# Kernel tuning notes

Measured on AMD Instinct MI355X. Metric: run time of the kernel, lower is better.

Reference implementation:

```python
import jax, jax.numpy as jnp
import numpy as np

RATE = 5          # negative_sample_rate
A = 1.0           # _a
BP = 1.0          # _b
REP = 1.0         # repulsion_strength
EPS = 1e-4        # clamp in compute_cross_entropy
BATCH = 65536; C = 100; E = 2048; GN = 16; GP = 5; NIDX = 50000


def setup_inputs() -> dict:
    key = jax.random.key(0)
    ks = jax.random.split(key, 12)
    return {
        'edge_to_idx': jax.random.randint(ks[0], (BATCH,), 0, NIDX),
        'edge_from_idx': jax.random.randint(ks[1], (BATCH,), 0, NIDX),
        'embedding_to': jax.random.normal(ks[2], (BATCH, 2), jnp.float32),
        'embedding_from': jax.random.normal(ks[3], (BATCH, 2), jnp.float32),
        'probs': jax.random.uniform(ks[4], (BATCH,), jnp.float32),
        'pred_edge_to': jax.random.normal(ks[5], (BATCH, C), jnp.float32),
        'pred_edge_from': jax.random.normal(ks[6], (BATCH, C), jnp.float32),
        'perm': jax.random.permutation(ks[7], BATCH * RATE),            # torch.randperm
        'error_conf': jnp.sort(jax.random.randint(ks[8], (E,), 0, NIDX)),
        'neg_grid': jax.random.normal(ks[9], (E, GN, 2), jnp.float32),
        'pos_grid': jax.random.normal(ks[10], (E, GP, 2), jnp.float32),
        'distance_list': jax.random.uniform(ks[11], (E,), jnp.float32),
    }


def _q(d):
    # convert_distance_to_probability: 1 / (1 + a * d^(2b))
    return 1.0 / (1.0 + A * d ** (2.0 * BP))


def _ce_attract(p, q):
    return -p * jnp.log(jnp.clip(q, EPS, 1.0))


def _ce_repulse(p, q):
    return -(1.0 - p) * REP * jnp.log(jnp.clip(1.0 - q, EPS, 1.0))


def _match(idx, error_conf):
    # first position in (sorted) error_conf equal to idx, plus hit mask
    pos = jnp.clip(jnp.searchsorted(error_conf, idx), 0, error_conf.shape[0] - 1)
    return pos, (error_conf[pos] == idx)


def reference(edge_to_idx, edge_from_idx, embedding_to, embedding_from, probs,
              pred_edge_to, pred_edge_from, perm, error_conf, neg_grid,
              pos_grid, distance_list):
    f32 = jnp.float32
    # ---- negative sampling (repeat_interleave + randperm) ----
    emb_neg_to = jnp.repeat(embedding_to, RATE, axis=0)         # [B*R,2]
    pred_neg_to = jnp.repeat(pred_edge_to, RATE, axis=0)        # [B*R,C]
    emb_neg_from = jnp.repeat(embedding_from, RATE, axis=0)[perm]
    pred_neg_from = jnp.repeat(pred_edge_from, RATE, axis=0)[perm]
    # filter_neg: keep where NOT (same argmax AND same max-softmax confidence)
    conf_from = jnp.max(jax.nn.softmax(pred_neg_from, axis=1), axis=1)
    conf_to = jnp.max(jax.nn.softmax(pred_neg_to, axis=1), axis=1)
    same = (jnp.argmax(pred_neg_from, axis=1) == jnp.argmax(pred_neg_to, axis=1)) & (conf_from == conf_to)
    m_neg = (~same).astype(f32)                                 # [B*R]
    neg_dist = jnp.linalg.norm(emb_neg_to - emb_neg_from, axis=1)
    neg_cnt = jnp.sum(m_neg)
    neg_mean = jnp.sum(neg_dist * m_neg) / jnp.maximum(neg_cnt, 1.0)
    # ---- positive distances ----
    pos_dist = jnp.linalg.norm(embedding_to - embedding_from, axis=1)  # [B]
    pos_mean = jnp.mean(pos_dist)
    # ---- confidence-grid pairs (vectorized isin/nonzero loops) ----
    g_to, hit_to = _match(edge_to_idx, error_conf)
    g_from, hit_from = _match(edge_from_idx, error_conf)
    m_to = hit_to.astype(f32)
    m_from = hit_from.astype(f32)
    d_cneg_to = jnp.linalg.norm(embedding_to[:, None, :] - neg_grid[g_to], axis=-1)     # [B,GN]
    d_cneg_from = jnp.linalg.norm(embedding_from[:, None, :] - neg_grid[g_from], axis=-1)
    d_cpos_to = jnp.linalg.norm(embedding_from[:, None, :] - pos_grid[g_to], axis=-1)   # [B,GP]
    d_cpos_from = jnp.linalg.norm(embedding_from[:, None, :] - pos_grid[g_from], axis=-1)
    w_pos_to = m_to * (distance_list[g_to] < 0.5).astype(f32)
    w_pos_from = m_from * (distance_list[g_from] < 1.0).astype(f32)
    # ---- UMAP cross entropy over the concatenated (pos, conf_pos, neg, conf_neg) ----
    ce_pos = _ce_attract(probs, _q(pos_dist)) + _ce_repulse(probs, _q(pos_dist))
    sum_ce = jnp.sum(ce_pos)
    sum_ce += jnp.sum(w_pos_to[:, None] * _ce_attract(1.0, _q(d_cpos_to)))
    sum_ce += jnp.sum(w_pos_from[:, None] * _ce_attract(1.0, _q(d_cpos_from)))
    sum_ce += jnp.sum(m_neg * _ce_repulse(0.0, _q(neg_dist)))
    sum_ce += jnp.sum(m_to[:, None] * _ce_repulse(0.0, _q(d_cneg_to)))
    sum_ce += jnp.sum(m_from[:, None] * _ce_repulse(0.0, _q(d_cneg_from)))
    total_cnt = (pos_dist.shape[0] + GP * (jnp.sum(w_pos_to) + jnp.sum(w_pos_from))
                 + neg_cnt + GN * (jnp.sum(m_to) + jnp.sum(m_from)))
    umap_l = sum_ce / jnp.maximum(total_cnt, 1.0)
    umap_l = jnp.where(jnp.isnan(umap_l), 0.0, umap_l)
    # ---- margin loss ----
    is_pred_same = (jnp.argmax(pred_edge_to, axis=1) == jnp.argmax(pred_edge_from, axis=1)).astype(f32)
    batch_margin = pos_mean + (neg_mean - pos_mean) * (1.0 - probs)
    margin = (1.0 - is_pred_same) * batch_margin
    margin_loss = jnp.mean(jax.nn.relu(margin - pos_dist))
    margin_loss = jnp.where(jnp.isnan(margin_loss), 0.0, margin_loss)
    return (umap_l, margin_loss, umap_l + margin_loss)


if __name__ == '__main__':
    out = reference(**setup_inputs())
    print([float(o) for o in out])
```

## Files before the change

### kernel.cpp

```cpp
#include <hip/hip_runtime.h>
#include <math.h>

#define B_SZ   65536
#define RATE   5
#define NNEG   (B_SZ * RATE)
#define NC     100
#define NE     2048
#define GN     16
#define GP     5
#define EPSC   1e-4f

#define NB_NEG 1280
#define NB_POS 256
#define NB_MAR 256


__device__ __forceinline__ double wave_sum(double v) {
    #pragma unroll
    for (int off = 32; off > 0; off >>= 1) v += __shfl_down(v, off, 64);
    return v;
}

__device__ __forceinline__ float clip01(float x) {
    return fminf(fmaxf(x, EPSC), 1.0f);
}

__global__ __launch_bounds__(256, 2) void k_rowstats(
    const float* __restrict__ pred_to, const float* __restrict__ pred_from,
    float* __restrict__ conf_to, float* __restrict__ conf_from,
    unsigned char* __restrict__ am_to, unsigned char* __restrict__ am_from)
{
    int i = blockIdx.x * blockDim.x + threadIdx.x;
    const float* row = (i < B_SZ) ? pred_to + (size_t)i * NC
                                  : pred_from + (size_t)(i - B_SZ) * NC;
    const float4* r4 = (const float4*)row;
    float4 v[25];
    #pragma unroll
    for (int t = 0; t < 25; ++t) v[t] = r4[t];

    float m = -INFINITY;
    #pragma unroll
    for (int t = 0; t < 25; ++t)
        m = fmaxf(m, fmaxf(fmaxf(v[t].x, v[t].y), fmaxf(v[t].z, v[t].w)));

    int bi = NC;
    float s = 0.0f;
    #pragma unroll
    for (int t = 0; t < 25; ++t) {
        float e0 = v[t].x, e1 = v[t].y, e2 = v[t].z, e3 = v[t].w;
        if (e0 == m) bi = min(bi, 4 * t + 0);
        if (e1 == m) bi = min(bi, 4 * t + 1);
        if (e2 == m) bi = min(bi, 4 * t + 2);
        if (e3 == m) bi = min(bi, 4 * t + 3);
        s += expf(e0 - m) + expf(e1 - m) + expf(e2 - m) + expf(e3 - m);
    }
    float conf = 1.0f / s;
    if (i < B_SZ) { conf_to[i] = conf;  am_to[i] = (unsigned char)bi; }
    else { conf_from[i - B_SZ] = conf; am_from[i - B_SZ] = (unsigned char)bi; }
}

__global__ __launch_bounds__(256) void k_negpos(
    const int* __restrict__ perm,
    const float2* __restrict__ emb_to, const float2* __restrict__ emb_from,
    const float* __restrict__ conf_to, const float* __restrict__ conf_from,
    const unsigned char* __restrict__ am_to, const unsigned char* __restrict__ am_from,
    const int* __restrict__ idx_to, const int* __restrict__ idx_from,
    const float* __restrict__ probs,
    const int* __restrict__ error_conf,
    const float2* __restrict__ neg_grid, const float2* __restrict__ pos_grid,
    const float* __restrict__ dist_list,
    double* __restrict__ pneg, double* __restrict__ ppos)
{
    if (blockIdx.x < NB_NEG) {
        int i = blockIdx.x * blockDim.x + threadIdx.x;
        double ce = 0.0, cnt = 0.0, dsum = 0.0;
        {
            int jt = i / RATE;
            int jf = perm[i] / RATE;
            bool same = (am_to[jt] == am_from[jf]) && (conf_to[jt] == conf_from[jf]);
            if (!same) {
                float2 et = emb_to[jt], ef = emb_from[jf];
                float dx = et.x - ef.x, dy = et.y - ef.y;
                float d  = sqrtf(dx * dx + dy * dy);
                float q  = 1.0f / (1.0f + d * d);
                ce   = (double)(-logf(clip01(1.0f - q)));
                cnt  = 1.0;
                dsum = (double)d;
            }
        }
        ce = wave_sum(ce); cnt = wave_sum(cnt); dsum = wave_sum(dsum);
        __shared__ double sr[3][4];
        int w = threadIdx.x >> 6;
        if ((threadIdx.x & 63) == 0) { sr[0][w] = ce; sr[1][w] = cnt; sr[2][w] = dsum; }
        __syncthreads();
        if (threadIdx.x == 0) {
            pneg[blockIdx.x * 3 + 0] = sr[0][0] + sr[0][1] + sr[0][2] + sr[0][3];
            pneg[blockIdx.x * 3 + 1] = sr[1][0] + sr[1][1] + sr[1][2] + sr[1][3];
            pneg[blockIdx.x * 3 + 2] = sr[2][0] + sr[2][1] + sr[2][2] + sr[2][3];
        }
    } else {
        int blk = blockIdx.x - NB_NEG;
        __shared__ int ec[NE];
        for (int t = threadIdx.x; t < NE; t += blockDim.x) ec[t] = error_conf[t];
        __syncthreads();

        int i = blk * blockDim.x + threadIdx.x;
        double v[6] = {0, 0, 0, 0, 0, 0};
        {
            float2 et = emb_to[i], ef = emb_from[i];
            float dx = et.x - ef.x, dy = et.y - ef.y;
            float d  = sqrtf(dx * dx + dy * dy);
            v[1] = (double)d;
            float p = probs[i];
            float q = 1.0f / (1.0f + d * d);
            double ce = (double)(-p * logf(clip01(q)) - (1.0f - p) * logf(clip01(1.0f - q)));

            int vt = idx_to[i];
            int lo = 0, hi = NE;
            while (lo < hi) { int mid = (lo + hi) >> 1; if (ec[mid] < vt) lo = mid + 1; else hi = mid; }
            int gt = (lo < NE) ? lo : NE - 1;
            bool hit_t = (ec[gt] == vt);

            int vf = idx_from[i];
            lo = 0; hi = NE;
            while (lo < hi) { int mid = (lo + hi) >> 1; if (ec[mid] < vf) lo = mid + 1; else hi = mid; }
            int gf = (lo < NE) ? lo : NE - 1;
            bool hit_f = (ec[gf] == vf);

            if (hit_t) {
                v[4] = 1.0;
                double s = 0.0;
                #pragma unroll
                for (int k = 0; k < GN; ++k) {
                    float2 g = neg_grid[gt * GN + k];
                    float ax = et.x - g.x, ay = et.y - g.y;
                    float dd = sqrtf(ax * ax + ay * ay);
                    float qq = 1.0f / (1.0f + dd * dd);
                    s += (double)(-logf(clip01(1.0f - qq)));
                }
                ce += s;
                if (dist_list[gt] < 0.5f) {
                    v[2] = 1.0;
                    double s2 = 0.0;
                    #pragma unroll
                    for (int k = 0; k < GP; ++k) {
                        float2 g = pos_grid[gt * GP + k];
                        float ax = ef.x - g.x, ay = ef.y - g.y;
                        float dd = sqrtf(ax * ax + ay * ay);
                        float qq = 1.0f / (1.0f + dd * dd);
                        s2 += (double)(-logf(clip01(qq)));
                    }
                    ce += s2;
                }
            }
            if (hit_f) {
                v[5] = 1.0;
                double s = 0.0;
                #pragma unroll
                for (int k = 0; k < GN; ++k) {
                    float2 g = neg_grid[gf * GN + k];
                    float ax = ef.x - g.x, ay = ef.y - g.y;
                    float dd = sqrtf(ax * ax + ay * ay);
                    float qq = 1.0f / (1.0f + dd * dd);
                    s += (double)(-logf(clip01(1.0f - qq)));
                }
                ce += s;
                if (dist_list[gf] < 1.0f) {
                    v[3] = 1.0;
                    double s2 = 0.0;
                    #pragma unroll
                    for (int k = 0; k < GP; ++k) {
                        float2 g = pos_grid[gf * GP + k];
                        float ax = ef.x - g.x, ay = ef.y - g.y;
                        float dd = sqrtf(ax * ax + ay * ay);
                        float qq = 1.0f / (1.0f + dd * dd);
                        s2 += (double)(-logf(clip01(qq)));
                    }
                    ce += s2;
                }
            }
            v[0] = ce;
        }
        __shared__ double sr2[6][4];
        int w = threadIdx.x >> 6;
        #pragma unroll
        for (int j = 0; j < 6; ++j) {
            double r = wave_sum(v[j]);
            if ((threadIdx.x & 63) == 0) sr2[j][w] = r;
        }
        __syncthreads();
        if (threadIdx.x < 6) {
            int j = threadIdx.x;
            ppos[blk * 6 + j] = sr2[j][0] + sr2[j][1] + sr2[j][2] + sr2[j][3];
        }
    }
}

__global__ __launch_bounds__(64) void k_reduce1(
    const double* __restrict__ pneg, const double* __restrict__ ppos,
    double* __restrict__ acc)
{
    int lane = threadIdx.x;
    double ce = 0.0, cnt = 0.0, dsum = 0.0;
    for (int b = lane; b < NB_NEG; b += 64) {
        ce   += pneg[b * 3 + 0];
        cnt  += pneg[b * 3 + 1];
        dsum += pneg[b * 3 + 2];
    }
    double pv[6] = {0, 0, 0, 0, 0, 0};
    for (int b = lane; b < NB_POS; b += 64) {
        #pragma unroll
        for (int j = 0; j < 6; ++j) pv[j] += ppos[b * 6 + j];
    }
    ce   = wave_sum(ce);
    cnt  = wave_sum(cnt);
    dsum = wave_sum(dsum);
    #pragma unroll
    for (int j = 0; j < 6; ++j) pv[j] = wave_sum(pv[j]);
    if (lane == 0) {
        acc[0] = ce + pv[0];
        acc[1] = cnt;
        acc[2] = dsum;
        acc[3] = pv[1];
        acc[4] = pv[2];
        acc[5] = pv[3];
        acc[6] = pv[4];
        acc[7] = pv[5];
    }
}

__global__ __launch_bounds__(256) void k_margin(
    const float2* __restrict__ emb_to, const float2* __restrict__ emb_from,
    const float* __restrict__ probs,
    const unsigned char* __restrict__ am_to, const unsigned char* __restrict__ am_from,
    const double* __restrict__ acc,
    double* __restrict__ pmar)
{
    int i = blockIdx.x * blockDim.x + threadIdx.x;
    float pos_mean = (float)(acc[3] / (double)B_SZ);
    float neg_mean = (float)(acc[2] / fmax(acc[1], 1.0));
    double ms;
    {
        float2 et = emb_to[i], ef = emb_from[i];
        float dx = et.x - ef.x, dy = et.y - ef.y;
        float d  = sqrtf(dx * dx + dy * dy);
        float p  = probs[i];
        float bm = pos_mean + (neg_mean - pos_mean) * (1.0f - p);
        float m  = (am_to[i] == am_from[i]) ? 0.0f : bm;
        ms = (double)fmaxf(m - d, 0.0f);
    }
    ms = wave_sum(ms);
    __shared__ double sr[4];
    int w = threadIdx.x >> 6;
    if ((threadIdx.x & 63) == 0) sr[w] = ms;
    __syncthreads();
    if (threadIdx.x == 0) pmar[blockIdx.x] = sr[0] + sr[1] + sr[2] + sr[3];
}

__global__ __launch_bounds__(64) void k_final(
    const double* __restrict__ acc, const double* __restrict__ pmar,
    float* __restrict__ out)
{
    int lane = threadIdx.x;
    double ms = 0.0;
    for (int b = lane; b < NB_MAR; b += 64) ms += pmar[b];
    ms = wave_sum(ms);
    if (lane == 0) {
        float sum_ce  = (float)acc[0];
        float neg_cnt = (float)acc[1];
        float total_cnt = (float)B_SZ
                        + (float)GP * ((float)acc[4] + (float)acc[5])
                        + neg_cnt
                        + (float)GN * ((float)acc[6] + (float)acc[7]);
        float umap = sum_ce / fmaxf(total_cnt, 1.0f);
        if (isnan(umap)) umap = 0.0f;
        float ml = (float)(ms / (double)B_SZ);
        if (isnan(ml)) ml = 0.0f;
        out[0] = umap;
        out[1] = ml;
        out[2] = umap + ml;
    }
}

extern "C" void kernel_launch(void* const* d_in, const int* in_sizes, int n_in,
                              void* d_out, int out_size, void* d_ws, size_t ws_size,
                              hipStream_t stream)
{
    const int*   edge_to_idx   = (const int*)d_in[0];
    const int*   edge_from_idx = (const int*)d_in[1];
    const float* embedding_to  = (const float*)d_in[2];
    const float* embedding_from= (const float*)d_in[3];
    const float* probs         = (const float*)d_in[4];
    const float* pred_to       = (const float*)d_in[5];
    const float* pred_from     = (const float*)d_in[6];
    const int*   perm          = (const int*)d_in[7];
    const int*   error_conf    = (const int*)d_in[8];
    const float* neg_grid      = (const float*)d_in[9];
    const float* pos_grid      = (const float*)d_in[10];
    const float* dist_list     = (const float*)d_in[11];

    char* ws = (char*)d_ws;
    double*        acc       = (double*)ws;
    float*         conf_to   = (float*)(ws + 128);
    float*         conf_from = conf_to + B_SZ;
    unsigned char* am_to     = (unsigned char*)(conf_from + B_SZ);
    unsigned char* am_from   = am_to + B_SZ;
    double*        pneg      = (double*)(am_from + B_SZ);
    double*        ppos      = pneg + NB_NEG * 3;
    double*        pmar      = ppos + NB_POS * 6;

    k_rowstats<<<(2 * B_SZ) / 256, 256, 0, stream>>>(
        pred_to, pred_from, conf_to, conf_from, am_to, am_from);

    k_negpos<<<NB_NEG + NB_POS, 256, 0, stream>>>(
        perm, (const float2*)embedding_to, (const float2*)embedding_from,
        conf_to, conf_from, am_to, am_from,
        edge_to_idx, edge_from_idx, probs, error_conf,
        (const float2*)neg_grid, (const float2*)pos_grid, dist_list,
        pneg, ppos);

    k_reduce1<<<1, 64, 0, stream>>>(pneg, ppos, acc);

    k_margin<<<NB_MAR, 256, 0, stream>>>(
        (const float2*)embedding_to, (const float2*)embedding_from,
        probs, am_to, am_from, acc, pmar);

    k_final<<<1, 64, 0, stream>>>(acc, pmar, (float*)d_out);
}
```

Baseline: 48.48 us.

## Fuse reduction kernels, pack row stats, and switch partial sums to float

Replaces the separate reduce and final kernels with one tail kernel. Every block there redundantly reduces the partials, and a last-block atomic counter finishes the output, removing two serialized single-block launches. Row confidence and argmax are packed into one 8-byte float2 so the negative-sample equality check is a single 64-bit gather. The negative and positive kernels now process four elements per thread with fewer blocks, and all accumulation moves from double to float with an algebraically simplified 1-q. The risks are reduced precision in the large sums and extra redundant partial reads in every tail block.

```diff
diff --git a/kernel.cpp b/kernel.cpp
--- a/kernel.cpp
+++ b/kernel.cpp
@@ -10,26 +10,25 @@
 #define GP     5
 #define EPSC   1e-4f
 
-#define NB_NEG 1280
-#define NB_POS 256
-#define NB_MAR 256
-
-
-__device__ __forceinline__ double wave_sum(double v) {
+#define NBN    320
+#define NBP    64
+#define NBT    256
+
+__device__ __forceinline__ float wave_sumf(float v) {
     #pragma unroll
     for (int off = 32; off > 0; off >>= 1) v += __shfl_down(v, off, 64);
     return v;
 }
-
 __device__ __forceinline__ float clip01(float x) {
     return fminf(fmaxf(x, EPSC), 1.0f);
 }
 
 __global__ __launch_bounds__(256, 2) void k_rowstats(
     const float* __restrict__ pred_to, const float* __restrict__ pred_from,
-    float* __restrict__ conf_to, float* __restrict__ conf_from,
-    unsigned char* __restrict__ am_to, unsigned char* __restrict__ am_from)
+    float2* __restrict__ pk_to, float2* __restrict__ pk_from,
+    unsigned int* __restrict__ counter)
 {
+    if (blockIdx.x == 0 && threadIdx.x == 0) *counter = 0u;
     int i = blockIdx.x * blockDim.x + threadIdx.x;
     const float* row = (i < B_SZ) ? pred_to + (size_t)i * NC
                                   : pred_from + (size_t)(i - B_SZ) * NC;
@@ -54,66 +53,67 @@
         if (e3 == m) bi = min(bi, 4 * t + 3);
         s += expf(e0 - m) + expf(e1 - m) + expf(e2 - m) + expf(e3 - m);
     }
-    float conf = 1.0f / s;
-    if (i < B_SZ) { conf_to[i] = conf;  am_to[i] = (unsigned char)bi; }
-    else { conf_from[i - B_SZ] = conf; am_from[i - B_SZ] = (unsigned char)bi; }
+    float2 pk = make_float2(1.0f / s, __uint_as_float((unsigned)bi));
+    if (i < B_SZ) pk_to[i] = pk; else pk_from[i - B_SZ] = pk;
 }
 
 __global__ __launch_bounds__(256) void k_negpos(
     const int* __restrict__ perm,
     const float2* __restrict__ emb_to, const float2* __restrict__ emb_from,
-    const float* __restrict__ conf_to, const float* __restrict__ conf_from,
-    const unsigned char* __restrict__ am_to, const unsigned char* __restrict__ am_from,
+    const float2* __restrict__ pk_to, const float2* __restrict__ pk_from,
     const int* __restrict__ idx_to, const int* __restrict__ idx_from,
     const float* __restrict__ probs,
     const int* __restrict__ error_conf,
     const float2* __restrict__ neg_grid, const float2* __restrict__ pos_grid,
     const float* __restrict__ dist_list,
-    double* __restrict__ pneg, double* __restrict__ ppos)
+    float* __restrict__ pneg, float* __restrict__ ppos)
 {
-    if (blockIdx.x < NB_NEG) {
-        int i = blockIdx.x * blockDim.x + threadIdx.x;
-        double ce = 0.0, cnt = 0.0, dsum = 0.0;
-        {
-            int jt = i / RATE;
-            int jf = perm[i] / RATE;
-            bool same = (am_to[jt] == am_from[jf]) && (conf_to[jt] == conf_from[jf]);
-            if (!same) {
+    __shared__ float sr[6][4];
+    int w = threadIdx.x >> 6, lane = threadIdx.x & 63;
+    if (blockIdx.x < NBN) {
+        const unsigned long long* pkt = (const unsigned long long*)pk_to;
+        const unsigned long long* pkf = (const unsigned long long*)pk_from;
+        int base = blockIdx.x * 1024 + threadIdx.x;
+        float ce = 0.f, cnt = 0.f, ds = 0.f;
+        #pragma unroll
+        for (int k = 0; k < 4; ++k) {
+            int i = base + k * 256;
+            unsigned jt = (unsigned)i / RATE;
+            unsigned jf = (unsigned)perm[i] / RATE;
+            if (pkt[jt] != pkf[jf]) {
                 float2 et = emb_to[jt], ef = emb_from[jf];
                 float dx = et.x - ef.x, dy = et.y - ef.y;
-                float d  = sqrtf(dx * dx + dy * dy);
-                float q  = 1.0f / (1.0f + d * d);
-                ce   = (double)(-logf(clip01(1.0f - q)));
-                cnt  = 1.0;
-                dsum = (double)d;
+                float d2 = dx * dx + dy * dy;
+                float om = d2 / (1.0f + d2);
+                ce  += -logf(clip01(om));
+                cnt += 1.0f;
+                ds  += sqrtf(d2);
             }
         }
-        ce = wave_sum(ce); cnt = wave_sum(cnt); dsum = wave_sum(dsum);
-        __shared__ double sr[3][4];
-        int w = threadIdx.x >> 6;
-        if ((threadIdx.x & 63) == 0) { sr[0][w] = ce; sr[1][w] = cnt; sr[2][w] = dsum; }
+        ce = wave_sumf(ce); cnt = wave_sumf(cnt); ds = wave_sumf(ds);
+        if (lane == 0) { sr[0][w] = ce; sr[1][w] = cnt; sr[2][w] = ds; }
         __syncthreads();
-        if (threadIdx.x == 0) {
-            pneg[blockIdx.x * 3 + 0] = sr[0][0] + sr[0][1] + sr[0][2] + sr[0][3];
-            pneg[blockIdx.x * 3 + 1] = sr[1][0] + sr[1][1] + sr[1][2] + sr[1][3];
-            pneg[blockIdx.x * 3 + 2] = sr[2][0] + sr[2][1] + sr[2][2] + sr[2][3];
+        if (threadIdx.x < 3) {
+            int j = threadIdx.x;
+            pneg[blockIdx.x * 3 + j] = sr[j][0] + sr[j][1] + sr[j][2] + sr[j][3];
         }
     } else {
-        int blk = blockIdx.x - NB_NEG;
         __shared__ int ec[NE];
-        for (int t = threadIdx.x; t < NE; t += blockDim.x) ec[t] = error_conf[t];
+        int blk = blockIdx.x - NBN;
+        for (int t = threadIdx.x; t < NE; t += 256) ec[t] = error_conf[t];
         __syncthreads();
 
-        int i = blk * blockDim.x + threadIdx.x;
-        double v[6] = {0, 0, 0, 0, 0, 0};
-        {
+        float v0 = 0.f, v1 = 0.f, v2 = 0.f, v3 = 0.f, v4 = 0.f, v5 = 0.f;
+        for (int k = 0; k < 4; ++k) {
+            int i = blk * 1024 + threadIdx.x + k * 256;
             float2 et = emb_to[i], ef = emb_from[i];
             float dx = et.x - ef.x, dy = et.y - ef.y;
-            float d  = sqrtf(dx * dx + dy * dy);
-            v[1] = (double)d;
+            float d2 = dx * dx + dy * dy;
+            v1 += sqrtf(d2);
             float p = probs[i];
-            float q = 1.0f / (1.0f + d * d);
-            double ce = (double)(-p * logf(clip01(q)) - (1.0f - p) * logf(clip01(1.0f - q)));
+            float q  = 1.0f / (1.0f + d2);
+            float om = d2 / (1.0f + d2);
+            v0 += -p * logf(clip01(q)) - (1.0f - p) * logf(clip01(om));
 
             int vt = idx_to[i];
             int lo = 0, hi = NE;
@@ -128,157 +128,142 @@
             bool hit_f = (ec[gf] == vf);
 
             if (hit_t) {
-                v[4] = 1.0;
-                double s = 0.0;
+                v4 += 1.0f;
+                float sa = 0.f;
                 #pragma unroll
-                for (int k = 0; k < GN; ++k) {
-                    float2 g = neg_grid[gt * GN + k];
+                for (int k2 = 0; k2 < GN; ++k2) {
+                    float2 g = neg_grid[gt * GN + k2];
                     float ax = et.x - g.x, ay = et.y - g.y;
-                    float dd = sqrtf(ax * ax + ay * ay);
-                    float qq = 1.0f / (1.0f + dd * dd);
-                    s += (double)(-logf(clip01(1.0f - qq)));
+                    float dd = ax * ax + ay * ay;
+                    sa += -logf(clip01(dd / (1.0f + dd)));
                 }
-                ce += s;
+                v0 += sa;
                 if (dist_list[gt] < 0.5f) {
-                    v[2] = 1.0;
-                    double s2 = 0.0;
+                    v2 += 1.0f;
+                    float s2 = 0.f;
                     #pragma unroll
-                    for (int k = 0; k < GP; ++k) {
-                        float2 g = pos_grid[gt * GP + k];
+                    for (int k2 = 0; k2 < GP; ++k2) {
+                        float2 g = pos_grid[gt * GP + k2];
                         float ax = ef.x - g.x, ay = ef.y - g.y;
-                        float dd = sqrtf(ax * ax + ay * ay);
-                        float qq = 1.0f / (1.0f + dd * dd);
-                        s2 += (double)(-logf(clip01(qq)));
+                        float dd = ax * ax + ay * ay;
+                        s2 += -logf(clip01(1.0f / (1.0f + dd)));
                     }
-                    ce += s2;
+                    v0 += s2;
                 }
             }
             if (hit_f) {
-                v[5] = 1.0;
-                double s = 0.0;
+                v5 += 1.0f;
+                float sa = 0.f;
                 #pragma unroll
-                for (int k = 0; k < GN; ++k) {
-                    float2 g = neg_grid[gf * GN + k];
+                for (int k2 = 0; k2 < GN; ++k2) {
+                    float2 g = neg_grid[gf * GN + k2];
                     float ax = ef.x - g.x, ay = ef.y - g.y;
-                    float dd = sqrtf(ax * ax + ay * ay);
-                    float qq = 1.0f / (1.0f + dd * dd);
-                    s += (double)(-logf(clip01(1.0f - qq)));
+                    float dd = ax * ax + ay * ay;
+                    sa += -logf(clip01(dd / (1.0f + dd)));
                 }
-                ce += s;
+                v0 += sa;
                 if (dist_list[gf] < 1.0f) {
-                    v[3] = 1.0;
-                    double s2 = 0.0;
+                    v3 += 1.0f;
+                    float s2 = 0.f;
                     #pragma unroll
-                    for (int k = 0; k < GP; ++k) {
-                        float2 g = pos_grid[gf * GP + k];
+                    for (int k2 = 0; k2 < GP; ++k2) {
+                        float2 g = pos_grid[gf * GP + k2];
                         float ax = ef.x - g.x, ay = ef.y - g.y;
-                        float dd = sqrtf(ax * ax + ay * ay);
-                        float qq = 1.0f / (1.0f + dd * dd);
-                        s2 += (double)(-logf(clip01(qq)));
+                        float dd = ax * ax + ay * ay;
+                        s2 += -logf(clip01(1.0f / (1.0f + dd)));
                     }
-                    ce += s2;
+                    v0 += s2;
                 }
             }
-            v[0] = ce;
-        }
-        __shared__ double sr2[6][4];
-        int w = threadIdx.x >> 6;
+        }
+        float vv[6] = {v0, v1, v2, v3, v4, v5};
         #pragma unroll
         for (int j = 0; j < 6; ++j) {
-            double r = wave_sum(v[j]);
-            if ((threadIdx.x & 63) == 0) sr2[j][w] = r;
+            float r = wave_sumf(vv[j]);
+            if (lane == 0) sr[j][w] = r;
         }
         __syncthreads();
         if (threadIdx.x < 6) {
             int j = threadIdx.x;
-            ppos[blk * 6 + j] = sr2[j][0] + sr2[j][1] + sr2[j][2] + sr2[j][3];
-        }
-    }
-}
-
-__global__ __launch_bounds__(64) void k_reduce1(
-    const double* __restrict__ pneg, const double* __restrict__ ppos,
-    double* __restrict__ acc)
-{
-    int lane = threadIdx.x;
-    double ce = 0.0, cnt = 0.0, dsum = 0.0;
-    for (int b = lane; b < NB_NEG; b += 64) {
-        ce   += pneg[b * 3 + 0];
-        cnt  += pneg[b * 3 + 1];
-        dsum += pneg[b * 3 + 2];
-    }
-    double pv[6] = {0, 0, 0, 0, 0, 0};
-    for (int b = lane; b < NB_POS; b += 64) {
-        #pragma unroll
-        for (int j = 0; j < 6; ++j) pv[j] += ppos[b * 6 + j];
-    }
-    ce   = wave_sum(ce);
-    cnt  = wave_sum(cnt);
-    dsum = wave_sum(dsum);
-    #pragma unroll
-    for (int j = 0; j < 6; ++j) pv[j] = wave_sum(pv[j]);
-    if (lane == 0) {
-        acc[0] = ce + pv[0];
-        acc[1] = cnt;
-        acc[2] = dsum;
-        acc[3] = pv[1];
-        acc[4] = pv[2];
-        acc[5] = pv[3];
-        acc[6] = pv[4];
-        acc[7] = pv[5];
-    }
-}
-
-__global__ __launch_bounds__(256) void k_margin(
+            ppos[blk * 6 + j] = sr[j][0] + sr[j][1] + sr[j][2] + sr[j][3];
+        }
+    }
+}
+
+__global__ __launch_bounds__(256) void k_tail(
     const float2* __restrict__ emb_to, const float2* __restrict__ emb_from,
     const float* __restrict__ probs,
-    const unsigned char* __restrict__ am_to, const unsigned char* __restrict__ am_from,
-    const double* __restrict__ acc,
-    double* __restrict__ pmar)
-{
-    int i = blockIdx.x * blockDim.x + threadIdx.x;
-    float pos_mean = (float)(acc[3] / (double)B_SZ);
-    float neg_mean = (float)(acc[2] / fmax(acc[1], 1.0));
-    double ms;
-    {
-        float2 et = emb_to[i], ef = emb_from[i];
-        float dx = et.x - ef.x, dy = et.y - ef.y;
-        float d  = sqrtf(dx * dx + dy * dy);
-        float p  = probs[i];
-        float bm = pos_mean + (neg_mean - pos_mean) * (1.0f - p);
-        float m  = (am_to[i] == am_from[i]) ? 0.0f : bm;
-        ms = (double)fmaxf(m - d, 0.0f);
-    }
-    ms = wave_sum(ms);
-    __shared__ double sr[4];
-    int w = threadIdx.x >> 6;
-    if ((threadIdx.x & 63) == 0) sr[w] = ms;
-    __syncthreads();
-    if (threadIdx.x == 0) pmar[blockIdx.x] = sr[0] + sr[1] + sr[2] + sr[3];
-}
-
-__global__ __launch_bounds__(64) void k_final(
-    const double* __restrict__ acc, const double* __restrict__ pmar,
+    const float2* __restrict__ pk_to, const float2* __restrict__ pk_from,
+    const float* __restrict__ pneg, const float* __restrict__ ppos,
+    float* __restrict__ pmar, unsigned int* __restrict__ counter,
     float* __restrict__ out)
 {
-    int lane = threadIdx.x;
-    double ms = 0.0;
-    for (int b = lane; b < NB_MAR; b += 64) ms += pmar[b];
-    ms = wave_sum(ms);
-    if (lane == 0) {
-        float sum_ce  = (float)acc[0];
-        float neg_cnt = (float)acc[1];
-        float total_cnt = (float)B_SZ
-                        + (float)GP * ((float)acc[4] + (float)acc[5])
-                        + neg_cnt
-                        + (float)GN * ((float)acc[6] + (float)acc[7]);
-        float umap = sum_ce / fmaxf(total_cnt, 1.0f);
-        if (isnan(umap)) umap = 0.0f;
-        float ml = (float)(ms / (double)B_SZ);
-        if (isnan(ml)) ml = 0.0f;
-        out[0] = umap;
-        out[1] = ml;
-        out[2] = umap + ml;
+    __shared__ float sr[8][4];
+    __shared__ float tot[8];
+    __shared__ bool islast;
+    int w = threadIdx.x >> 6, lane = threadIdx.x & 63;
+
+    float s[8] = {0, 0, 0, 0, 0, 0, 0, 0};
+    for (int b = threadIdx.x; b < NBN; b += 256) {
+        s[0] += pneg[b * 3 + 0]; s[1] += pneg[b * 3 + 1]; s[2] += pneg[b * 3 + 2];
+    }
+    if (threadIdx.x < NBP) {
+        int b = threadIdx.x;
+        s[0] += ppos[b * 6 + 0]; s[3] += ppos[b * 6 + 1]; s[4] += ppos[b * 6 + 2];
+        s[5] += ppos[b * 6 + 3]; s[6] += ppos[b * 6 + 4]; s[7] += ppos[b * 6 + 5];
+    }
+    #pragma unroll
+    for (int j = 0; j < 8; ++j) {
+        float r = wave_sumf(s[j]);
+        if (lane == 0) sr[j][w] = r;
+    }
+    __syncthreads();
+    if (threadIdx.x < 8) {
+        int j = threadIdx.x;
+        tot[j] = sr[j][0] + sr[j][1] + sr[j][2] + sr[j][3];
+    }
+    __syncthreads();
+    float pos_mean = tot[3] * (1.0f / (float)B_SZ);
+    float neg_mean = tot[2] / fmaxf(tot[1], 1.0f);
+
+    int i = blockIdx.x * 256 + threadIdx.x;
+    float2 et = emb_to[i], ef = emb_from[i];
+    float2 at = pk_to[i], af = pk_from[i];
+    float dx = et.x - ef.x, dy = et.y - ef.y;
+    float d = sqrtf(dx * dx + dy * dy);
+    float p = probs[i];
+    float bm = pos_mean + (neg_mean - pos_mean) * (1.0f - p);
+    float mg = (at.y == af.y) ? 0.0f : bm;
+    float ms = fmaxf(mg - d, 0.0f);
+    ms = wave_sumf(ms);
+    if (lane == 0) sr[0][w] = ms;
+    __syncthreads();
+
+    if (threadIdx.x == 0) {
+        pmar[blockIdx.x] = sr[0][0] + sr[0][1] + sr[0][2] + sr[0][3];
+        __threadfence();
+        unsigned old = atomicAdd(counter, 1u);
+        islast = (old == NBT - 1);
+    }
+    __syncthreads();
+    if (islast) {
+        __threadfence();
+        float v = pmar[threadIdx.x];
+        v = wave_sumf(v);
+        if (lane == 0) sr[1][w] = v;
+        __syncthreads();
+        if (threadIdx.x == 0) {
+            float msum = sr[1][0] + sr[1][1] + sr[1][2] + sr[1][3];
+            float total_cnt = (float)B_SZ + (float)GP * (tot[4] + tot[5])
+                            + tot[1] + (float)GN * (tot[6] + tot[7]);
+            float umap = tot[0] / fmaxf(total_cnt, 1.0f);
+            if (isnan(umap)) umap = 0.0f;
+            float ml = msum * (1.0f / (float)B_SZ);
+            if (isnan(ml)) ml = 0.0f;
+            out[0] = umap;
+            out[1] = ml;
+            out[2] = umap + ml;
+        }
     }
 }
 
@@ -300,30 +285,24 @@
     const float* dist_list     = (const float*)d_in[11];
 
     char* ws = (char*)d_ws;
-    double*        acc       = (double*)ws;
-    float*         conf_to   = (float*)(ws + 128);
-    float*         conf_from = conf_to + B_SZ;
-    unsigned char* am_to     = (unsigned char*)(conf_from + B_SZ);
-    unsigned char* am_from   = am_to + B_SZ;
-    double*        pneg      = (double*)(am_from + B_SZ);
-    double*        ppos      = pneg + NB_NEG * 3;
-    double*        pmar      = ppos + NB_POS * 6;
+    unsigned int* counter = (unsigned int*)ws;
+    float2*       pk_to   = (float2*)(ws + 256);
+    float2*       pk_from = pk_to + B_SZ;
+    float*        pneg    = (float*)(pk_from + B_SZ);
+    float*        ppos    = pneg + NBN * 3;
+    float*        pmar    = ppos + NBP * 6;
 
     k_rowstats<<<(2 * B_SZ) / 256, 256, 0, stream>>>(
-        pred_to, pred_from, conf_to, conf_from, am_to, am_from);
-
-    k_negpos<<<NB_NEG + NB_POS, 256, 0, stream>>>(
+        pred_to, pred_from, pk_to, pk_from, counter);
+
+    k_negpos<<<NBN + NBP, 256, 0, stream>>>(
         perm, (const float2*)embedding_to, (const float2*)embedding_from,
-        conf_to, conf_from, am_to, am_from,
+        pk_to, pk_from,
         edge_to_idx, edge_from_idx, probs, error_conf,
         (const float2*)neg_grid, (const float2*)pos_grid, dist_list,
         pneg, ppos);
 
-    k_reduce1<<<1, 64, 0, stream>>>(pneg, ppos, acc);
-
-    k_margin<<<NB_MAR, 256, 0, stream>>>(
+    k_tail<<<NBT, 256, 0, stream>>>(
         (const float2*)embedding_to, (const float2*)embedding_from,
-        probs, am_to, am_from, acc, pmar);
-
-    k_final<<<1, 64, 0, stream>>>(acc, pmar, (float*)d_out);
-}
+        probs, pk_to, pk_from, pneg, ppos, pmar, counter, (float*)d_out);
+}
```

Result: slower. 66.16 us (+36.5%).
